# Kernel tuning notes

Measured on AMD Instinct MI355X. Metric: run time of the kernel, lower is better.

The kernel has to match this reference:

```python
import jax, jax.numpy as jnp
import numpy as np

GROUPS = 32
EPS = 1e-5
NUM_HEADS = 8
HEAD_DIM = 64
CHANNELS = 512


def group_norm(x, scale, bias):
    # x: [b, h, w, c]; normalize over (h, w, channels-within-group)
    b, h, w, c = x.shape
    xg = x.reshape(b, h, w, GROUPS, c // GROUPS)
    mean = jnp.mean(xg, axis=(1, 2, 4), keepdims=True)
    var = jnp.var(xg, axis=(1, 2, 4), keepdims=True)
    xg = (xg - mean) * jax.lax.rsqrt(var + EPS)
    return xg.reshape(b, h, w, c) * scale + bias


def setup_inputs() -> dict:
    key = jax.random.key(0)
    ks = jax.random.split(key, 8)
    b, hs, ws, c = 8, 32, 32, CHANNELS
    inner = NUM_HEADS * HEAD_DIM
    return {
        "x": jax.random.normal(ks[0], (b, hs, ws, c), dtype=jnp.float32),
        "t": jax.random.normal(ks[1], (b,), dtype=jnp.float32),
        "gn_scale": jnp.ones((c,), dtype=jnp.float32),
        "gn_bias": jnp.zeros((c,), dtype=jnp.float32),
        "w_qkv": jax.random.normal(ks[2], (c, 3 * inner), dtype=jnp.float32) * 0.02,
        "b_qkv": jnp.zeros((3 * inner,), dtype=jnp.float32),
        "w_out": jax.random.normal(ks[3], (inner, c), dtype=jnp.float32) * 0.02,
        "b_out": jnp.zeros((c,), dtype=jnp.float32),
    }


def reference(x, t, gn_scale, gn_bias, w_qkv, b_qkv, w_out, b_out):
    b, hs, ws, c = x.shape
    # NOTE: original reassigns x = GroupNorm(x); the residual uses the NORMALIZED x.
    xn = group_norm(x, gn_scale, gn_bias)
    x_flat = xn.reshape(b, hs * ws, c)                      # [b, s, c]
    qkv = x_flat @ w_qkv + b_qkv                            # [b, s, 3*nh*hd]
    qkv = qkv.reshape(b, hs * ws, NUM_HEADS, 3 * HEAD_DIM)
    q, k, v = jnp.split(qkv, 3, axis=-1)                    # each [b, s, nh, hd]
    q = q / jnp.sqrt(jnp.float32(HEAD_DIM))
    q = q.transpose(0, 2, 1, 3)                             # [b, nh, s, hd]
    k = k.transpose(0, 2, 1, 3)
    v = v.transpose(0, 2, 1, 3)
    attn = jax.nn.softmax(jnp.einsum('bhqd,bhkd->bhqk', q, k), axis=-1)
    out = jnp.einsum('bhqk,bhkd->bhqd', attn, v)            # [b, nh, s, hd]
    out = out.transpose(0, 2, 1, 3).reshape(b, hs * ws, NUM_HEADS * HEAD_DIM)
    h = out @ w_out + b_out                                 # [b, s, c]
    h = h.reshape(b, hs, ws, c)
    return xn + h
```

## Files before the change

kernel.cpp:

```cpp
#include <hip/hip_runtime.h>
#include <hip/hip_bf16.h>


#define B_    8
#define S_    1024
#define C_    512
#define NH    8
#define HD    64
#define QKVC  1536
#define GROUPS 32
#define GSIZE  16
#define EPSV   1e-5f
#define QSCL  0.18033688f

using frag8 = __attribute__((ext_vector_type(8))) short;
using f32x4 = __attribute__((ext_vector_type(4))) float;

__device__ __forceinline__ float bf2f(unsigned short u) {
    union { unsigned int i; float f; } v; v.i = ((unsigned int)u) << 16; return v.f;
}
__device__ __forceinline__ unsigned short f2bf(float f) {
    union { float f; unsigned int i; } v; v.f = f;
    unsigned int x = v.i;
    return (unsigned short)((x + 0x7fffu + ((x >> 16) & 1u)) >> 16);
}
__device__ __forceinline__ unsigned int pk2bf(float a, float b) {
    union { float f; unsigned int u; } x, y; x.f = a; y.f = b;
    return __builtin_amdgcn_perm(y.u + 0x8000u, x.u + 0x8000u, 0x07060302u);
}
__device__ __forceinline__ float fexp2(float x) {
#if __has_builtin(__builtin_amdgcn_exp2f)
    return __builtin_amdgcn_exp2f(x);
#else
    return exp2f(x);
#endif
}
__device__ __forceinline__ f32x4 zero4() {
    f32x4 z; z[0] = 0.f; z[1] = 0.f; z[2] = 0.f; z[3] = 0.f; return z;
}
__device__ __forceinline__ void gl_lds(const unsigned short* gp, unsigned short* lp) {
    __builtin_amdgcn_global_load_lds(
        (const __attribute__((address_space(1))) void*)gp,
        (__attribute__((address_space(3))) void*)lp, 16, 0, 0);
}

__global__ __launch_bounds__(256) void transpose_kernel(
        const float* __restrict__ in, unsigned short* __restrict__ out,
        int K, int N) {
    __shared__ float tile[32][33];
    int n0 = blockIdx.x * 32, k0 = blockIdx.y * 32;
    int t = threadIdx.x;
    for (int i = 0; i < 4; ++i) {
        int idx = t + i * 256; int r = idx >> 5, c = idx & 31;
        tile[r][c] = in[(size_t)(k0 + r) * N + n0 + c];
    }
    __syncthreads();
    for (int i = 0; i < 4; ++i) {
        int idx = t + i * 256; int r = idx >> 5, c = idx & 31;
        out[(size_t)(n0 + r) * K + k0 + c] = f2bf(tile[c][r]);
    }
}

__global__ __launch_bounds__(256) void gn_kernel(
        const float* __restrict__ x,
        const float* __restrict__ scale,
        const float* __restrict__ bias,
        unsigned short* __restrict__ xn) {
    int bg = blockIdx.x;
    int b = bg >> 5, g = bg & 31;
    const float* xb = x + (size_t)b * S_ * C_;
    int t = threadIdx.x;

    float sum = 0.f, ss = 0.f;
    for (int i = 0; i < 16; ++i) {
        int idx = t + i * 256;
        int row = idx >> 2, j = idx & 3;
        float4 v = *(const float4*)(xb + (size_t)row * C_ + g * GSIZE + j * 4);
        sum += v.x + v.y + v.z + v.w;
        ss  += v.x * v.x + v.y * v.y + v.z * v.z + v.w * v.w;
    }
    for (int off = 1; off < 64; off <<= 1) {
        sum += __shfl_xor(sum, off);
        ss  += __shfl_xor(ss,  off);
    }
    __shared__ float s_sum[4], s_ss[4];
    int wid = t >> 6;
    if ((t & 63) == 0) { s_sum[wid] = sum; s_ss[wid] = ss; }
    __syncthreads();
    sum = s_sum[0] + s_sum[1] + s_sum[2] + s_sum[3];
    ss  = s_ss[0]  + s_ss[1]  + s_ss[2]  + s_ss[3];
    float mean = sum * (1.f / 16384.f);
    float var  = ss * (1.f / 16384.f) - mean * mean;
    float rinv = rsqrtf(var + EPSV);

    float sc[16], bi[16];
    for (int u = 0; u < 16; ++u) {
        sc[u] = scale[g * GSIZE + u];
        bi[u] = bias[g * GSIZE + u];
    }
    for (int i = 0; i < 16; ++i) {
        int idx = t + i * 256;
        int row = idx >> 2, j = idx & 3;
        float4 v = *(const float4*)(xb + (size_t)row * C_ + g * GSIZE + j * 4);
        int c0 = j * 4;
        float f0 = (v.x - mean) * rinv * sc[c0 + 0] + bi[c0 + 0];
        float f1 = (v.y - mean) * rinv * sc[c0 + 1] + bi[c0 + 1];
        float f2 = (v.z - mean) * rinv * sc[c0 + 2] + bi[c0 + 2];
        float f3 = (v.w - mean) * rinv * sc[c0 + 3] + bi[c0 + 3];
        uint2 o;
        o.x = (unsigned int)f2bf(f0) | ((unsigned int)f2bf(f1) << 16);
        o.y = (unsigned int)f2bf(f2) | ((unsigned int)f2bf(f3) << 16);
        *(uint2*)(xn + (size_t)b * S_ * C_ + (size_t)row * C_ + g * GSIZE + c0) = o;
    }
}

template<int MODE>
__global__ __launch_bounds__(256) void gemm_kernel(
        const unsigned short* __restrict__ A,
        const unsigned short* __restrict__ Bt,
        const float* __restrict__ bias,
        const unsigned short* __restrict__ resid,
        unsigned short* __restrict__ outA,
        unsigned short* __restrict__ outV,
        float* __restrict__ outF,
        int M, int N, int K) {
    __shared__ unsigned short As[2][128 * 32];
    __shared__ unsigned short Bs[2][128 * 32];
    int m0 = blockIdx.y * 128, n0 = blockIdx.x * 128;
    int t = threadIdx.x;
    int wid = t >> 6, lane = t & 63;
    int quad = lane >> 4, l16 = lane & 15;
    int wm = (wid >> 1) * 64, wn = (wid & 1) * 64;

    f32x4 acc[4][4];
    for (int mi = 0; mi < 4; ++mi)
        for (int ni = 0; ni < 4; ++ni) acc[mi][ni] = zero4();

    int srow = t >> 2, sseg = t & 3;
    auto stage = [&](int k0, int buf) {
        for (int i = 0; i < 2; ++i) {
            gl_lds(A + (size_t)(m0 + i * 64 + srow) * K + k0 + sseg * 8,
                   &As[buf][(size_t)(i * 256 + wid * 64) * 8]);
            gl_lds(Bt + (size_t)(n0 + i * 64 + srow) * K + k0 + sseg * 8,
                   &Bs[buf][(size_t)(i * 256 + wid * 64) * 8]);
        }
    };

    stage(0, 0);
    int nk = K >> 5;
    for (int i = 0; i < nk; ++i) {
        __syncthreads();
        if (i + 1 < nk) stage((i + 1) << 5, (i + 1) & 1);
        int buf = i & 1;

        frag8 bfrag[4], afrag[4];
        for (int ni = 0; ni < 4; ++ni)
            bfrag[ni] = *(const frag8*)(&Bs[buf][(wn + ni * 16 + l16) * 32 + quad * 8]);
        for (int mi = 0; mi < 4; ++mi)
            afrag[mi] = *(const frag8*)(&As[buf][(wm + mi * 16 + l16) * 32 + quad * 8]);

        for (int mi = 0; mi < 4; ++mi)
            for (int ni = 0; ni < 4; ++ni)
                acc[mi][ni] = __builtin_amdgcn_mfma_f32_16x16x32_bf16(
                    afrag[mi], bfrag[ni], acc[mi][ni], 0, 0, 0);
    }

    for (int ni = 0; ni < 4; ++ni) {
        int c0 = n0 + wn + ni * 16;
        float bv = bias[c0 + l16];
        if (MODE == 0) {
            int h = c0 / 192, rr = c0 % 192;
            if (rr >= 128) {
                int d = rr - 128 + l16;
                int bidx = m0 >> 10;
                unsigned short* vp = outV + (((size_t)bidx * NH + h) * HD + d) * S_
                                   + (m0 & 1023) + wm + quad * 4;
                for (int mi = 0; mi < 4; ++mi) {
                    uint2 pk;
                    pk.x = pk2bf(acc[mi][ni][0] + bv, acc[mi][ni][1] + bv);
                    pk.y = pk2bf(acc[mi][ni][2] + bv, acc[mi][ni][3] + bv);
                    *(uint2*)(vp + mi * 16) = pk;
                }
            } else {
                float scl = (rr < 64) ? QSCL : 1.0f;
                int colk = h * 128 + rr + l16;
                for (int mi = 0; mi < 4; ++mi)
                    for (int r = 0; r < 4; ++r) {
                        int row = m0 + wm + mi * 16 + quad * 4 + r;
                        outA[(size_t)row * 1024 + colk] = f2bf((acc[mi][ni][r] + bv) * scl);
                    }
            }
        } else {
            int col = c0 + l16;
            for (int mi = 0; mi < 4; ++mi)
                for (int r = 0; r < 4; ++r) {
                    int row = m0 + wm + mi * 16 + quad * 4 + r;
                    float v = acc[mi][ni][r] + bv + bf2f(resid[(size_t)row * N + col]);
                    outF[(size_t)row * N + col] = v;
                }
        }
    }
}

__global__ __launch_bounds__(256) void attn_kernel(
        const unsigned short* __restrict__ kq,
        const unsigned short* __restrict__ vT,
        unsigned short* __restrict__ attn_out) {
    int i = blockIdx.x;
    int xcd = i & 7, slot = i >> 3;
    int bh = xcd * 8 + (slot >> 3);
    int qt = slot & 7;
    int b = bh >> 3, h = bh & 7;

    int t = threadIdx.x;
    int wid = t >> 6, lane = t & 63, quad = lane >> 4, l16 = lane & 15;
    int q0 = qt * 128 + wid * 32;

    __shared__ unsigned short Ks[2][2048];
    __shared__ unsigned short Vs[2][2048];
    __shared__ unsigned short Ps[4][32 * 40];

    frag8 qf[2][2];
    for (int mi = 0; mi < 2; ++mi) {
        const unsigned short* qrow = kq + ((size_t)b * S_ + q0 + mi * 16 + l16) * 1024 + h * 128;
        qf[mi][0] = *(const frag8*)(qrow + quad * 8);
        qf[mi][1] = *(const frag8*)(qrow + 32 + quad * 8);
    }
    frag8 ones;
    for (int i2 = 0; i2 < 8; ++i2) ones[i2] = (short)0x3f80;

    f32x4 o[2][4], ol[2];
    for (int mi = 0; mi < 2; ++mi) {
        ol[mi] = zero4();
        for (int dt = 0; dt < 4; ++dt) o[mi][dt] = zero4();
    }

    const unsigned short* kbase = kq + (size_t)b * S_ * 1024 + h * 128 + 64;
    const unsigned short* vbase = vT + ((size_t)b * NH + h) * HD * S_;
    unsigned short* pw = &Ps[wid][0];

    int kdh = wid & 1, krh = wid >> 1;
    int krow = krh * 16 + (lane >> 2);
    int kseg = lane & 3;
    int vd = wid * 16 + (lane >> 2);
    int vseg = lane & 3;

    auto stage = [&](int j0, int buf) {
        gl_lds(kbase + (size_t)(j0 + krow) * 1024 + kdh * 32 + kseg * 8,
               &Ks[buf][kdh * 1024 + krh * 512]);
        gl_lds(vbase + (size_t)vd * S_ + j0 + vseg * 8,
               &Vs[buf][wid * 512]);
    };

    stage(0, 0);

    for (int it = 0; it < S_ / 32; ++it) {
        int cur = it & 1, nxt = cur ^ 1;
        __syncthreads();
        if (it < S_ / 32 - 1) stage((it + 1) * 32, nxt);

        frag8 kf[2][2];
        for (int kh = 0; kh < 2; ++kh)
            for (int dh = 0; dh < 2; ++dh)
                kf[kh][dh] = *(const frag8*)(&Ks[cur][dh * 1024 + (kh * 16 + l16) * 32 + quad * 8]);

        f32x4 s[2][2];
        for (int mi = 0; mi < 2; ++mi)
            for (int kh = 0; kh < 2; ++kh) {
                f32x4 acc = zero4();
                acc = __builtin_amdgcn_mfma_f32_16x16x32_bf16(kf[kh][0], qf[mi][0], acc, 0, 0, 0);
                acc = __builtin_amdgcn_mfma_f32_16x16x32_bf16(kf[kh][1], qf[mi][1], acc, 0, 0, 0);
                s[mi][kh] = acc;
            }

        for (int mi = 0; mi < 2; ++mi)
            for (int kh = 0; kh < 2; ++kh) {
                float p0 = fexp2(s[mi][kh][0]);
                float p1 = fexp2(s[mi][kh][1]);
                float p2 = fexp2(s[mi][kh][2]);
                float p3 = fexp2(s[mi][kh][3]);
                uint2 pk;
                pk.x = pk2bf(p0, p1);
                pk.y = pk2bf(p2, p3);
                *(uint2*)(&pw[(mi * 16 + l16) * 40 + kh * 16 + quad * 4]) = pk;
            }

        frag8 pf[2];
        pf[0] = *(const frag8*)(&pw[l16 * 40 + quad * 8]);
        pf[1] = *(const frag8*)(&pw[(16 + l16) * 40 + quad * 8]);

        frag8 vf[4];
        for (int dt = 0; dt < 4; ++dt)
            vf[dt] = *(const frag8*)(&Vs[cur][(dt * 16 + l16) * 32 + quad * 8]);

        for (int mi = 0; mi < 2; ++mi) {
            ol[mi] = __builtin_amdgcn_mfma_f32_16x16x32_bf16(pf[mi], ones, ol[mi], 0, 0, 0);
            for (int dt = 0; dt < 4; ++dt)
                o[mi][dt] = __builtin_amdgcn_mfma_f32_16x16x32_bf16(pf[mi], vf[dt], o[mi][dt], 0, 0, 0);
        }
    }

    for (int mi = 0; mi < 2; ++mi)
        for (int r = 0; r < 4; ++r) {
            float inv = 1.0f / ol[mi][r];
            int qrw = q0 + mi * 16 + quad * 4 + r;
            for (int dt = 0; dt < 4; ++dt) {
                int ch = h * HD + dt * 16 + l16;
                attn_out[((size_t)b * S_ + qrw) * C_ + ch] = f2bf(o[mi][dt][r] * inv);
            }
        }
}

extern "C" void kernel_launch(void* const* d_in, const int* in_sizes, int n_in,
                              void* d_out, int out_size, void* d_ws, size_t ws_size,
                              hipStream_t stream) {
    const float* x        = (const float*)d_in[0];
    const float* gn_scale = (const float*)d_in[2];
    const float* gn_bias  = (const float*)d_in[3];
    const float* w_qkv    = (const float*)d_in[4];
    const float* b_qkv    = (const float*)d_in[5];
    const float* w_out    = (const float*)d_in[6];
    const float* b_out    = (const float*)d_in[7];
    float* out = (float*)d_out;

    char* ws = (char*)d_ws;
    unsigned short* xn    = (unsigned short*)(ws);
    unsigned short* kq    = (unsigned short*)(ws + ((size_t)8  << 20));
    unsigned short* attn  = (unsigned short*)(ws + ((size_t)24 << 20));
    unsigned short* vT    = (unsigned short*)(ws + ((size_t)32 << 20));
    unsigned short* wqkvT = (unsigned short*)(ws + ((size_t)40 << 20));
    unsigned short* woutT = (unsigned short*)(ws + ((size_t)40 << 20) + ((size_t)3 << 19));

    transpose_kernel<<<dim3(QKVC / 32, C_ / 32), 256, 0, stream>>>(w_qkv, wqkvT, C_, QKVC);
    transpose_kernel<<<dim3(C_ / 32, C_ / 32), 256, 0, stream>>>(w_out, woutT, C_, C_);

    gn_kernel<<<dim3(B_ * GROUPS), 256, 0, stream>>>(x, gn_scale, gn_bias, xn);

    gemm_kernel<0><<<dim3(QKVC / 128, (B_ * S_) / 128), 256, 0, stream>>>(
        xn, wqkvT, b_qkv, nullptr, kq, vT, nullptr, B_ * S_, QKVC, C_);

    attn_kernel<<<dim3(512), 256, 0, stream>>>(kq, vT, attn);

    gemm_kernel<1><<<dim3(C_ / 128, (B_ * S_) / 128), 256, 0, stream>>>(
        attn, woutT, b_out, xn, nullptr, nullptr, out, B_ * S_, C_, C_);
}
```

Before: 170.7 us.

## Halve attention query tile to double grid size and merge weight transposes

The attention kernel now gives each wave 16 query rows instead of 32, so each block covers 64 queries and the grid grows from 512 to 1024 blocks. This is meant to raise occupancy and CU utilization on a GPU with many CUs. The cost is that each staged K/V tile is reused by half as many queries, doubling total K/V traffic through LDS and L2. The two weight-transpose launches are also merged into a single kernel to save one launch.

```diff
diff --git a/kernel.cpp b/kernel.cpp
--- a/kernel.cpp
+++ b/kernel.cpp
@@ -44,11 +44,14 @@
         (__attribute__((address_space(3))) void*)lp, 16, 0, 0);
 }
 
-__global__ __launch_bounds__(256) void transpose_kernel(
-        const float* __restrict__ in, unsigned short* __restrict__ out,
-        int K, int N) {
+__global__ __launch_bounds__(256) void transpose2_kernel(
+        const float* __restrict__ w_qkv, const float* __restrict__ w_out,
+        unsigned short* __restrict__ wqkvT, unsigned short* __restrict__ woutT) {
     __shared__ float tile[32][33];
-    int n0 = blockIdx.x * 32, k0 = blockIdx.y * 32;
+    int id = blockIdx.x;
+    const float* in; unsigned short* out; int N, n0, k0;
+    if (id < 768) { in = w_qkv; out = wqkvT; N = QKVC; n0 = (id % 48) * 32; k0 = (id / 48) * 32; }
+    else { id -= 768; in = w_out; out = woutT; N = C_; n0 = (id % 16) * 32; k0 = (id / 16) * 32; }
     int t = threadIdx.x;
     for (int i = 0; i < 4; ++i) {
         int idx = t + i * 256; int r = idx >> 5, c = idx & 31;
@@ -57,7 +60,7 @@
     __syncthreads();
     for (int i = 0; i < 4; ++i) {
         int idx = t + i * 256; int r = idx >> 5, c = idx & 31;
-        out[(size_t)(n0 + r) * K + k0 + c] = f2bf(tile[c][r]);
+        out[(size_t)(n0 + r) * C_ + k0 + c] = f2bf(tile[c][r]);
     }
 }
 
@@ -208,32 +211,28 @@
         unsigned short* __restrict__ attn_out) {
     int i = blockIdx.x;
     int xcd = i & 7, slot = i >> 3;
-    int bh = xcd * 8 + (slot >> 3);
-    int qt = slot & 7;
+    int bh = xcd * 8 + (slot >> 4);
+    int qt = slot & 15;
     int b = bh >> 3, h = bh & 7;
 
     int t = threadIdx.x;
     int wid = t >> 6, lane = t & 63, quad = lane >> 4, l16 = lane & 15;
-    int q0 = qt * 128 + wid * 32;
+    int q0 = qt * 64 + wid * 16;
 
     __shared__ unsigned short Ks[2][2048];
     __shared__ unsigned short Vs[2][2048];
-    __shared__ unsigned short Ps[4][32 * 40];
-
-    frag8 qf[2][2];
-    for (int mi = 0; mi < 2; ++mi) {
-        const unsigned short* qrow = kq + ((size_t)b * S_ + q0 + mi * 16 + l16) * 1024 + h * 128;
-        qf[mi][0] = *(const frag8*)(qrow + quad * 8);
-        qf[mi][1] = *(const frag8*)(qrow + 32 + quad * 8);
-    }
+    __shared__ unsigned short Ps[4][16 * 40];
+
+    const unsigned short* qrow = kq + ((size_t)b * S_ + q0 + l16) * 1024 + h * 128;
+    frag8 qf0 = *(const frag8*)(qrow + quad * 8);
+    frag8 qf1 = *(const frag8*)(qrow + 32 + quad * 8);
+
     frag8 ones;
     for (int i2 = 0; i2 < 8; ++i2) ones[i2] = (short)0x3f80;
 
-    f32x4 o[2][4], ol[2];
-    for (int mi = 0; mi < 2; ++mi) {
-        ol[mi] = zero4();
-        for (int dt = 0; dt < 4; ++dt) o[mi][dt] = zero4();
-    }
+    f32x4 o[4], ol;
+    ol = zero4();
+    for (int dt = 0; dt < 4; ++dt) o[dt] = zero4();
 
     const unsigned short* kbase = kq + (size_t)b * S_ * 1024 + h * 128 + 64;
     const unsigned short* vbase = vT + ((size_t)b * NH + h) * HD * S_;
@@ -264,51 +263,44 @@
             for (int dh = 0; dh < 2; ++dh)
                 kf[kh][dh] = *(const frag8*)(&Ks[cur][dh * 1024 + (kh * 16 + l16) * 32 + quad * 8]);
 
-        f32x4 s[2][2];
-        for (int mi = 0; mi < 2; ++mi)
-            for (int kh = 0; kh < 2; ++kh) {
-                f32x4 acc = zero4();
-                acc = __builtin_amdgcn_mfma_f32_16x16x32_bf16(kf[kh][0], qf[mi][0], acc, 0, 0, 0);
-                acc = __builtin_amdgcn_mfma_f32_16x16x32_bf16(kf[kh][1], qf[mi][1], acc, 0, 0, 0);
-                s[mi][kh] = acc;
-            }
-
-        for (int mi = 0; mi < 2; ++mi)
-            for (int kh = 0; kh < 2; ++kh) {
-                float p0 = fexp2(s[mi][kh][0]);
-                float p1 = fexp2(s[mi][kh][1]);
-                float p2 = fexp2(s[mi][kh][2]);
-                float p3 = fexp2(s[mi][kh][3]);
-                uint2 pk;
-                pk.x = pk2bf(p0, p1);
-                pk.y = pk2bf(p2, p3);
-                *(uint2*)(&pw[(mi * 16 + l16) * 40 + kh * 16 + quad * 4]) = pk;
-            }
-
-        frag8 pf[2];
-        pf[0] = *(const frag8*)(&pw[l16 * 40 + quad * 8]);
-        pf[1] = *(const frag8*)(&pw[(16 + l16) * 40 + quad * 8]);
+        f32x4 s[2];
+        for (int kh = 0; kh < 2; ++kh) {
+            f32x4 acc = zero4();
+            acc = __builtin_amdgcn_mfma_f32_16x16x32_bf16(kf[kh][0], qf0, acc, 0, 0, 0);
+            acc = __builtin_amdgcn_mfma_f32_16x16x32_bf16(kf[kh][1], qf1, acc, 0, 0, 0);
+            s[kh] = acc;
+        }
+
+        for (int kh = 0; kh < 2; ++kh) {
+            float p0 = fexp2(s[kh][0]);
+            float p1 = fexp2(s[kh][1]);
+            float p2 = fexp2(s[kh][2]);
+            float p3 = fexp2(s[kh][3]);
+            uint2 pk;
+            pk.x = pk2bf(p0, p1);
+            pk.y = pk2bf(p2, p3);
+            *(uint2*)(&pw[l16 * 40 + kh * 16 + quad * 4]) = pk;
+        }
+
+        frag8 pf = *(const frag8*)(&pw[l16 * 40 + quad * 8]);
 
         frag8 vf[4];
         for (int dt = 0; dt < 4; ++dt)
             vf[dt] = *(const frag8*)(&Vs[cur][(dt * 16 + l16) * 32 + quad * 8]);
 
-        for (int mi = 0; mi < 2; ++mi) {
-            ol[mi] = __builtin_amdgcn_mfma_f32_16x16x32_bf16(pf[mi], ones, ol[mi], 0, 0, 0);
-            for (int dt = 0; dt < 4; ++dt)
-                o[mi][dt] = __builtin_amdgcn_mfma_f32_16x16x32_bf16(pf[mi], vf[dt], o[mi][dt], 0, 0, 0);
-        }
-    }
-
-    for (int mi = 0; mi < 2; ++mi)
-        for (int r = 0; r < 4; ++r) {
-            float inv = 1.0f / ol[mi][r];
-            int qrw = q0 + mi * 16 + quad * 4 + r;
-            for (int dt = 0; dt < 4; ++dt) {
-                int ch = h * HD + dt * 16 + l16;
-                attn_out[((size_t)b * S_ + qrw) * C_ + ch] = f2bf(o[mi][dt][r] * inv);
-            }
-        }
+        ol = __builtin_amdgcn_mfma_f32_16x16x32_bf16(pf, ones, ol, 0, 0, 0);
+        for (int dt = 0; dt < 4; ++dt)
+            o[dt] = __builtin_amdgcn_mfma_f32_16x16x32_bf16(pf, vf[dt], o[dt], 0, 0, 0);
+    }
+
+    for (int r = 0; r < 4; ++r) {
+        float inv = 1.0f / ol[r];
+        int qrw = q0 + quad * 4 + r;
+        for (int dt = 0; dt < 4; ++dt) {
+            int ch = h * HD + dt * 16 + l16;
+            attn_out[((size_t)b * S_ + qrw) * C_ + ch] = f2bf(o[dt][r] * inv);
+        }
+    }
 }
 
 extern "C" void kernel_launch(void* const* d_in, const int* in_sizes, int n_in,
@@ -331,15 +323,14 @@
     unsigned short* wqkvT = (unsigned short*)(ws + ((size_t)40 << 20));
     unsigned short* woutT = (unsigned short*)(ws + ((size_t)40 << 20) + ((size_t)3 << 19));
 
-    transpose_kernel<<<dim3(QKVC / 32, C_ / 32), 256, 0, stream>>>(w_qkv, wqkvT, C_, QKVC);
-    transpose_kernel<<<dim3(C_ / 32, C_ / 32), 256, 0, stream>>>(w_out, woutT, C_, C_);
+    transpose2_kernel<<<dim3(1024), 256, 0, stream>>>(w_qkv, w_out, wqkvT, woutT);
 
     gn_kernel<<<dim3(B_ * GROUPS), 256, 0, stream>>>(x, gn_scale, gn_bias, xn);
 
     gemm_kernel<0><<<dim3(QKVC / 128, (B_ * S_) / 128), 256, 0, stream>>>(
         xn, wqkvT, b_qkv, nullptr, kq, vT, nullptr, B_ * S_, QKVC, C_);
 
-    attn_kernel<<<dim3(512), 256, 0, stream>>>(kq, vT, attn);
+    attn_kernel<<<dim3(1024), 256, 0, stream>>>(kq, vT, attn);
 
     gemm_kernel<1><<<dim3(C_ / 128, (B_ * S_) / 128), 256, 0, stream>>>(
         attn, woutT, b_out, xn, nullptr, nullptr, out, B_ * S_, C_, C_);
```

Result: faster. 164.8 us (-3.5%).
